# Performance work log

Measured on AMD Instinct MI355X. Metric: run time of the kernel, lower is better.

Reference implementation:

```python
import jax, jax.numpy as jnp
import numpy as np

N_NODES = 50000
N_EDGES = 800000
IN_CH = 256
OUT_CH = 64
HEADS = 4
NEG_SLOPE = 0.2


def setup_inputs() -> dict:
    key = jax.random.key(0)
    k = jax.random.split(key, 7)
    x = jax.random.normal(k[0], (N_NODES, IN_CH), dtype=jnp.float32)
    edge_index = jax.random.randint(k[1], (2, N_EDGES), 0, N_NODES, dtype=jnp.int32)
    # Glorot-style init for the linear projection and attention vectors
    W = jax.random.normal(k[2], (IN_CH, HEADS * OUT_CH), dtype=jnp.float32) / np.sqrt(IN_CH)
    att_src = jax.random.normal(k[3], (HEADS, OUT_CH), dtype=jnp.float32) / np.sqrt(OUT_CH)
    att_dst = jax.random.normal(k[4], (HEADS, OUT_CH), dtype=jnp.float32) / np.sqrt(OUT_CH)
    bias = jnp.zeros((HEADS * OUT_CH,), dtype=jnp.float32)
    return {"x": x, "edge_index": edge_index, "W": W,
            "att_src": att_src, "att_dst": att_dst, "bias": bias}


def reference(x, edge_index, W, att_src, att_dst, bias):
    N = x.shape[0]
    # PyG GATConv default: add self-loops
    loop = jnp.arange(N, dtype=edge_index.dtype)
    src = jnp.concatenate([edge_index[0], loop])
    dst = jnp.concatenate([edge_index[1], loop])

    h = (x @ W).reshape(N, HEADS, OUT_CH)          # [N,H,C]
    a_src = jnp.einsum('nhc,hc->nh', h, att_src)    # [N,H]
    a_dst = jnp.einsum('nhc,hc->nh', h, att_dst)    # [N,H]

    alpha = a_src[src] + a_dst[dst]                 # [E,H]
    alpha = jax.nn.leaky_relu(alpha, NEG_SLOPE)

    # segment softmax over edges grouped by destination node
    amax = jax.ops.segment_max(alpha, dst, num_segments=N)
    amax = jnp.where(jnp.isfinite(amax), amax, 0.0)
    e = jnp.exp(alpha - amax[dst])
    denom = jax.ops.segment_sum(e, dst, num_segments=N)
    coef = e / (denom[dst] + 1e-16)                 # [E,H]

    msg = coef[..., None] * h[src]                  # [E,H,C]
    out = jax.ops.segment_sum(msg, dst, num_segments=N)  # [N,H,C]
    out = out.reshape(N, HEADS * OUT_CH) + bias
    return jax.nn.relu(out)
```

## Files before the change

### kernel.cpp

```cpp
#include <hip/hip_runtime.h>
#include <hip/hip_bf16.h>

#define HC 256
#define NEG_SLOPE 0.2f
#define BM 64
#define BK 64
#define LDK 72

typedef short short8_t __attribute__((ext_vector_type(8)));
typedef float float4_t __attribute__((ext_vector_type(4)));

__device__ __forceinline__ unsigned short f2bf(float f) {
  unsigned u = __float_as_uint(f);
  return (unsigned short)((u + 0x7fffu + ((u >> 16) & 1u)) >> 16);
}
__device__ __forceinline__ float bf2f(unsigned short b) {
  return __uint_as_float(((unsigned)b) << 16);
}

__global__ void wt_kernel(const float* __restrict__ W, unsigned short* __restrict__ Wt)
{
  const int k = blockIdx.x;
  const int n = threadIdx.x;
  Wt[n * 256 + k] = f2bf(W[k * 256 + n]);
}

__global__ __launch_bounds__(256) void gemm_mfma(
    const float* __restrict__ x, const unsigned short* __restrict__ Wt,
    const float* __restrict__ att_src, const float* __restrict__ att_dst,
    unsigned short* __restrict__ h, float* __restrict__ a_src,
    float* __restrict__ a_dst, int nnodes)
{
  __shared__ unsigned short As[BM * LDK];
  __shared__ unsigned short Bs[256 * LDK];
  const int t    = threadIdx.x;
  const int wv   = t >> 6;
  const int lane = t & 63;
  const int r0   = blockIdx.x * BM;

  float4_t acc[4][4] = {};

  for (int k0 = 0; k0 < 256; k0 += BK) {
    __syncthreads();
    {
      const int row = t >> 2, kc = (t & 3) * 16;
      const int gr = r0 + row;
      float4 xv[4];
      if (gr < nnodes) {
        const float4* p = (const float4*)(x + (size_t)gr * 256 + k0 + kc);
        xv[0] = p[0]; xv[1] = p[1]; xv[2] = p[2]; xv[3] = p[3];
      } else {
        xv[0] = xv[1] = xv[2] = xv[3] = make_float4(0.f, 0.f, 0.f, 0.f);
      }
      const float* f = (const float*)xv;
      unsigned pk[8];
      #pragma unroll
      for (int i = 0; i < 8; ++i) {
        __hip_bfloat162 b2 = __float22bfloat162_rn(make_float2(f[2 * i], f[2 * i + 1]));
        pk[i] = *(unsigned*)&b2;
      }
      uint4* d = (uint4*)&As[row * LDK + kc];
      d[0] = make_uint4(pk[0], pk[1], pk[2], pk[3]);
      d[1] = make_uint4(pk[4], pk[5], pk[6], pk[7]);
    }
    #pragma unroll
    for (int it = 0; it < 4; ++it) {
      const int n = it * 64 + (t >> 2);
      const int kc = (t & 3) * 16;
      const uint4* g = (const uint4*)(Wt + (size_t)n * 256 + k0 + kc);
      uint4 v0 = g[0], v1 = g[1];
      uint4* d = (uint4*)&Bs[n * LDK + kc];
      d[0] = v0; d[1] = v1;
    }
    __syncthreads();

    #pragma unroll
    for (int ks = 0; ks < 2; ++ks) {
      const int ko = ks * 32 + (lane >> 4) * 8;
      short8_t af[4], bfr[4];
      #pragma unroll
      for (int mt = 0; mt < 4; ++mt)
        af[mt] = *(const short8_t*)&As[(16 * mt + (lane & 15)) * LDK + ko];
      #pragma unroll
      for (int nt = 0; nt < 4; ++nt)
        bfr[nt] = *(const short8_t*)&Bs[(64 * wv + 16 * nt + (lane & 15)) * LDK + ko];
      #pragma unroll
      for (int mt = 0; mt < 4; ++mt)
        #pragma unroll
        for (int nt = 0; nt < 4; ++nt)
          acc[mt][nt] = __builtin_amdgcn_mfma_f32_16x16x32_bf16(
              af[mt], bfr[nt], acc[mt][nt], 0, 0, 0);
    }
  }

  const int q = lane >> 4, l15 = lane & 15;
  float atts[4], attd[4];
  #pragma unroll
  for (int nt = 0; nt < 4; ++nt) {
    atts[nt] = att_src[wv * 64 + 16 * nt + l15];
    attd[nt] = att_dst[wv * 64 + 16 * nt + l15];
  }

  #pragma unroll
  for (int mt = 0; mt < 4; ++mt) {
    #pragma unroll
    for (int reg = 0; reg < 4; ++reg) {
      const int row = r0 + 16 * mt + 4 * q + reg;
      const bool ok = row < nnodes;
      float ps = 0.f, pd = 0.f;
      #pragma unroll
      for (int nt = 0; nt < 4; ++nt) {
        const float v = acc[mt][nt][reg];
        if (ok) h[(size_t)row * 256 + 64 * wv + 16 * nt + l15] = f2bf(v);
        ps += v * atts[nt];
        pd += v * attd[nt];
      }
      #pragma unroll
      for (int off = 8; off; off >>= 1) {
        ps += __shfl_down(ps, off, 16);
        pd += __shfl_down(pd, off, 16);
      }
      if (ok && l15 == 0) {
        a_src[row * 4 + wv] = ps;
        a_dst[row * 4 + wv] = pd;
      }
    }
  }
}

__global__ void deg_count(const int* __restrict__ ei, int* __restrict__ deg, int E)
{
  const int e = blockIdx.x * blockDim.x + threadIdx.x;
  if (e >= E) return;
  atomicAdd(&deg[ei[E + e]], 1);
}

__global__ __launch_bounds__(256) void scan_p1(const int* __restrict__ deg,
                                               int* __restrict__ bsum, int n)
{
  __shared__ int ws[4];
  const int t = threadIdx.x, lane = t & 63, wv = t >> 6;
  const int base = blockIdx.x * 1024 + t * 4;
  int4 v = make_int4(0, 0, 0, 0);
  if (base + 3 < n) v = *(const int4*)&deg[base];
  else {
    if (base + 0 < n) v.x = deg[base + 0];
    if (base + 1 < n) v.y = deg[base + 1];
    if (base + 2 < n) v.z = deg[base + 2];
  }
  int s = (v.x + v.y) + (v.z + v.w);
  #pragma unroll
  for (int off = 32; off; off >>= 1) s += __shfl_down(s, off, 64);
  if (lane == 0) ws[wv] = s;
  __syncthreads();
  if (t == 0) bsum[blockIdx.x] = (ws[0] + ws[1]) + (ws[2] + ws[3]);
}

__global__ __launch_bounds__(1024) void scan_p2(const int* __restrict__ bsum,
                                                int* __restrict__ boff,
                                                int* __restrict__ rowptr,
                                                int nb, int n)
{
  __shared__ int wsum[16], woff[16];
  const int t = threadIdx.x, lane = t & 63, wv = t >> 6;
  int v = (t < nb) ? bsum[t] : 0;
  int sc = v;
  #pragma unroll
  for (int off = 1; off < 64; off <<= 1) {
    int u = __shfl_up(sc, off, 64);
    if (lane >= off) sc += u;
  }
  if (lane == 63) wsum[wv] = sc;
  __syncthreads();
  if (t == 0) {
    int run = 0;
    #pragma unroll
    for (int i = 0; i < 16; ++i) { int x = wsum[i]; woff[i] = run; run += x; }
    rowptr[n] = run;
  }
  __syncthreads();
  if (t < nb) boff[t] = woff[wv] + sc - v;
}

__global__ __launch_bounds__(256) void scan_p3(const int* __restrict__ deg,
                                               const int* __restrict__ boff,
                                               int* __restrict__ rowptr,
                                               int* __restrict__ cursor, int n)
{
  __shared__ int wsum[4], woff[4];
  const int t = threadIdx.x, lane = t & 63, wv = t >> 6;
  const int base = blockIdx.x * 1024 + t * 4;
  int4 v = make_int4(0, 0, 0, 0);
  if (base + 3 < n) v = *(const int4*)&deg[base];
  else {
    if (base + 0 < n) v.x = deg[base + 0];
    if (base + 1 < n) v.y = deg[base + 1];
    if (base + 2 < n) v.z = deg[base + 2];
  }
  const int s = (v.x + v.y) + (v.z + v.w);
  int sc = s;
  #pragma unroll
  for (int off = 1; off < 64; off <<= 1) {
    int u = __shfl_up(sc, off, 64);
    if (lane >= off) sc += u;
  }
  if (lane == 63) wsum[wv] = sc;
  __syncthreads();
  if (t == 0) {
    int run = 0;
    #pragma unroll
    for (int i = 0; i < 4; ++i) { int x = wsum[i]; woff[i] = run; run += x; }
  }
  __syncthreads();
  int excl = boff[blockIdx.x] + woff[wv] + (sc - s);
  int4 r;
  r.x = excl;
  r.y = r.x + v.x;
  r.z = r.y + v.y;
  r.w = r.z + v.z;
  if (base + 3 < n) {
    *(int4*)&rowptr[base] = r;
    *(int4*)&cursor[base] = r;
  } else {
    if (base + 0 < n) { rowptr[base + 0] = r.x; cursor[base + 0] = r.x; }
    if (base + 1 < n) { rowptr[base + 1] = r.y; cursor[base + 1] = r.y; }
    if (base + 2 < n) { rowptr[base + 2] = r.z; cursor[base + 2] = r.z; }
  }
}

__global__ __launch_bounds__(256) void fill_csr(
    const int* __restrict__ ei, const float* __restrict__ a_src,
    const float* __restrict__ a_dst, int* __restrict__ cursor,
    int* __restrict__ csr_src, float4* __restrict__ wexp, int E, int nnodes)
{
  const int g    = blockIdx.x & 7;
  const int bg   = blockIdx.x >> 3;
  const int nbg  = gridDim.x >> 3;
  const int gsz  = (nnodes + 7) >> 3;
  const int dlo  = g * gsz;
  const int dhi  = min(dlo + gsz, nnodes);

  for (int e = bg * 256 + threadIdx.x; e < E; e += nbg * 256) {
    const int d = ei[E + e];
    if (d < dlo || d >= dhi) continue;
    const int s = ei[e];
    const int pos = atomicAdd(&cursor[d], 1);
    csr_src[pos] = s;
    const float4 as = ((const float4*)a_src)[s];
    const float4 ad = ((const float4*)a_dst)[d];
    float4 al;
    al.x = as.x + ad.x; al.y = as.y + ad.y;
    al.z = as.z + ad.z; al.w = as.w + ad.w;
    al.x = al.x > 0.f ? al.x : NEG_SLOPE * al.x;
    al.y = al.y > 0.f ? al.y : NEG_SLOPE * al.y;
    al.z = al.z > 0.f ? al.z : NEG_SLOPE * al.z;
    al.w = al.w > 0.f ? al.w : NEG_SLOPE * al.w;
    al.x = expf(al.x); al.y = expf(al.y); al.z = expf(al.z); al.w = expf(al.w);
    wexp[pos] = al;
  }
}

__device__ __forceinline__ float4 ld_h(const unsigned short* __restrict__ h,
                                       int row, int cb)
{
  const ushort4 u = *(const ushort4*)&h[(size_t)row * 256 + cb];
  return make_float4(bf2f(u.x), bf2f(u.y), bf2f(u.z), bf2f(u.w));
}

__global__ __launch_bounds__(256) void gather_kernel(
    const int* __restrict__ rowptr, const int* __restrict__ csr_src,
    const float* __restrict__ wexp, const unsigned short* __restrict__ h,
    const float* __restrict__ a_src, const float* __restrict__ a_dst,
    const float* __restrict__ bias, float* __restrict__ out, int n)
{
  const int wave = threadIdx.x >> 6;
  const int lane = threadIdx.x & 63;
  const int d = blockIdx.x * 4 + wave;
  if (d >= n) return;

  const int head = lane >> 4;
  const int cb   = lane * 4;

  float alpha = a_src[d * 4 + head] + a_dst[d * 4 + head];
  alpha = alpha > 0.f ? alpha : NEG_SLOPE * alpha;
  float w = expf(alpha);
  float dsum = w;
  float4 hv = ld_h(h, d, cb);
  float4 acc = make_float4(w * hv.x, w * hv.y, w * hv.z, w * hv.w);

  int j = rowptr[d];
  const int end = rowptr[d + 1];

  for (; j + 3 < end; j += 4) {
    const int4 s4 = *(const int4*)&csr_src[j];
    const float w0 = wexp[(j + 0) * 4 + head];
    const float w1 = wexp[(j + 1) * 4 + head];
    const float w2 = wexp[(j + 2) * 4 + head];
    const float w3 = wexp[(j + 3) * 4 + head];
    const float4 h0 = ld_h(h, s4.x, cb);
    const float4 h1 = ld_h(h, s4.y, cb);
    const float4 h2 = ld_h(h, s4.z, cb);
    const float4 h3 = ld_h(h, s4.w, cb);
    dsum += (w0 + w1) + (w2 + w3);
    acc.x += w0 * h0.x + w1 * h1.x + w2 * h2.x + w3 * h3.x;
    acc.y += w0 * h0.y + w1 * h1.y + w2 * h2.y + w3 * h3.y;
    acc.z += w0 * h0.z + w1 * h1.z + w2 * h2.z + w3 * h3.z;
    acc.w += w0 * h0.w + w1 * h1.w + w2 * h2.w + w3 * h3.w;
  }
  for (; j < end; ++j) {
    const int s0 = csr_src[j];
    const float w0 = wexp[j * 4 + head];
    const float4 h0 = ld_h(h, s0, cb);
    dsum += w0;
    acc.x += w0 * h0.x; acc.y += w0 * h0.y;
    acc.z += w0 * h0.z; acc.w += w0 * h0.w;
  }

  const float inv = 1.f / (dsum + 1e-16f);
  const float4 b4 = ((const float4*)bias)[lane];
  float4 o;
  o.x = acc.x * inv + b4.x; o.x = o.x > 0.f ? o.x : 0.f;
  o.y = acc.y * inv + b4.y; o.y = o.y > 0.f ? o.y : 0.f;
  o.z = acc.z * inv + b4.z; o.z = o.z > 0.f ? o.z : 0.f;
  o.w = acc.w * inv + b4.w; o.w = o.w > 0.f ? o.w : 0.f;
  *(float4*)&out[(size_t)d * 256 + cb] = o;
}

extern "C" void kernel_launch(void* const* d_in, const int* in_sizes, int n_in,
                              void* d_out, int out_size, void* d_ws, size_t ws_size,
                              hipStream_t stream)
{
  const float* x       = (const float*)d_in[0];
  const int*   ei      = (const int*)d_in[1];
  const float* W       = (const float*)d_in[2];
  const float* att_src = (const float*)d_in[3];
  const float* att_dst = (const float*)d_in[4];
  const float* bias    = (const float*)d_in[5];

  const int nnodes = in_sizes[0] / HC;
  const int E      = in_sizes[1] / 2;
  const int nb     = (nnodes + 1023) / 1024;

  float* out = (float*)d_out;
  char* ws = (char*)d_ws;
  unsigned short* h  = (unsigned short*)ws;
  float* a_src = (float*)(ws + (size_t)nnodes * HC * 2);
  float* a_dst = a_src + (size_t)nnodes * 4;
  unsigned short* Wt = (unsigned short*)(a_dst + (size_t)nnodes * 4);
  int* deg    = (int*)((char*)Wt + 256 * 256 * 2);
  int* rowptr = deg + nnodes;
  int* cursor = rowptr + ((nnodes + 1 + 3) & ~3);
  int* bsum   = cursor + nnodes;
  int* boff   = bsum + ((nb + 3) & ~3);
  float4* wexp = (float4*)(boff + ((nb + 3) & ~3));
  int* csr    = (int*)(wexp + E);

  hipMemsetAsync(deg, 0, (size_t)nnodes * sizeof(int), stream);

  wt_kernel<<<256, 256, 0, stream>>>(W, Wt);

  gemm_mfma<<<(nnodes + BM - 1) / BM, 256, 0, stream>>>(
      x, Wt, att_src, att_dst, h, a_src, a_dst, nnodes);

  deg_count<<<(E + 255) / 256, 256, 0, stream>>>(ei, deg, E);
  scan_p1<<<nb, 256, 0, stream>>>(deg, bsum, nnodes);
  scan_p2<<<1, 1024, 0, stream>>>(bsum, boff, rowptr, nb, nnodes);
  scan_p3<<<nb, 256, 0, stream>>>(deg, boff, rowptr, cursor, nnodes);

  fill_csr<<<1024, 256, 0, stream>>>(ei, a_src, a_dst, cursor, csr,
                                     (float4*)wexp, E, nnodes);

  gather_kernel<<<(nnodes + 3) / 4, 256, 0, stream>>>(
      rowptr, csr, (const float*)wexp, h, a_src, a_dst, bias, out, nnodes);
}
```

Baseline: 276.7 us.

## Fuse degree count into GEMM launch, enlarge GEMM tile, vectorize CSR fill and unroll gather

```diff
diff --git a/kernel.cpp b/kernel.cpp
--- a/kernel.cpp
+++ b/kernel.cpp
@@ -3,7 +3,7 @@
 
 #define HC 256
 #define NEG_SLOPE 0.2f
-#define BM 64
+#define BM 128
 #define BK 64
 #define LDK 72
 
@@ -25,43 +25,62 @@
   Wt[n * 256 + k] = f2bf(W[k * 256 + n]);
 }
 
-__global__ __launch_bounds__(256) void gemm_mfma(
+__global__ __launch_bounds__(256) void gemm_deg(
     const float* __restrict__ x, const unsigned short* __restrict__ Wt,
     const float* __restrict__ att_src, const float* __restrict__ att_dst,
     unsigned short* __restrict__ h, float* __restrict__ a_src,
-    float* __restrict__ a_dst, int nnodes)
+    float* __restrict__ a_dst, const int* __restrict__ ei,
+    int* __restrict__ deg, int E, int nnodes, int degBlocks)
 {
   __shared__ unsigned short As[BM * LDK];
   __shared__ unsigned short Bs[256 * LDK];
-  const int t    = threadIdx.x;
+  const int t = threadIdx.x;
+
+  if (blockIdx.x < degBlocks) {
+    const int base = (blockIdx.x * 256 + t) * 4;
+    if (base + 3 < E) {
+      const int4 d4 = *(const int4*)&ei[E + base];
+      atomicAdd(&deg[d4.x], 1);
+      atomicAdd(&deg[d4.y], 1);
+      atomicAdd(&deg[d4.z], 1);
+      atomicAdd(&deg[d4.w], 1);
+    } else {
+      for (int e = base; e < E; ++e) atomicAdd(&deg[ei[E + e]], 1);
+    }
+    return;
+  }
+
   const int wv   = t >> 6;
   const int lane = t & 63;
-  const int r0   = blockIdx.x * BM;
-
-  float4_t acc[4][4] = {};
+  const int r0   = (blockIdx.x - degBlocks) * BM;
+
+  float4_t acc[8][4] = {};
 
   for (int k0 = 0; k0 < 256; k0 += BK) {
     __syncthreads();
     {
-      const int row = t >> 2, kc = (t & 3) * 16;
+      const int row = t >> 1, kc = (t & 1) * 32;
       const int gr = r0 + row;
-      float4 xv[4];
+      float4 xv[8];
       if (gr < nnodes) {
         const float4* p = (const float4*)(x + (size_t)gr * 256 + k0 + kc);
-        xv[0] = p[0]; xv[1] = p[1]; xv[2] = p[2]; xv[3] = p[3];
+        #pragma unroll
+        for (int i = 0; i < 8; ++i) xv[i] = p[i];
       } else {
-        xv[0] = xv[1] = xv[2] = xv[3] = make_float4(0.f, 0.f, 0.f, 0.f);
+        #pragma unroll
+        for (int i = 0; i < 8; ++i) xv[i] = make_float4(0.f, 0.f, 0.f, 0.f);
       }
       const float* f = (const float*)xv;
-      unsigned pk[8];
-      #pragma unroll
-      for (int i = 0; i < 8; ++i) {
+      unsigned pk[16];
+      #pragma unroll
+      for (int i = 0; i < 16; ++i) {
         __hip_bfloat162 b2 = __float22bfloat162_rn(make_float2(f[2 * i], f[2 * i + 1]));
         pk[i] = *(unsigned*)&b2;
       }
       uint4* d = (uint4*)&As[row * LDK + kc];
-      d[0] = make_uint4(pk[0], pk[1], pk[2], pk[3]);
-      d[1] = make_uint4(pk[4], pk[5], pk[6], pk[7]);
+      #pragma unroll
+      for (int i = 0; i < 4; ++i)
+        d[i] = make_uint4(pk[4 * i], pk[4 * i + 1], pk[4 * i + 2], pk[4 * i + 3]);
     }
     #pragma unroll
     for (int it = 0; it < 4; ++it) {
@@ -77,15 +96,15 @@
     #pragma unroll
     for (int ks = 0; ks < 2; ++ks) {
       const int ko = ks * 32 + (lane >> 4) * 8;
-      short8_t af[4], bfr[4];
-      #pragma unroll
-      for (int mt = 0; mt < 4; ++mt)
-        af[mt] = *(const short8_t*)&As[(16 * mt + (lane & 15)) * LDK + ko];
+      short8_t af[8], bfr[4];
       #pragma unroll
       for (int nt = 0; nt < 4; ++nt)
         bfr[nt] = *(const short8_t*)&Bs[(64 * wv + 16 * nt + (lane & 15)) * LDK + ko];
       #pragma unroll
-      for (int mt = 0; mt < 4; ++mt)
+      for (int mt = 0; mt < 8; ++mt)
+        af[mt] = *(const short8_t*)&As[(16 * mt + (lane & 15)) * LDK + ko];
+      #pragma unroll
+      for (int mt = 0; mt < 8; ++mt)
         #pragma unroll
         for (int nt = 0; nt < 4; ++nt)
           acc[mt][nt] = __builtin_amdgcn_mfma_f32_16x16x32_bf16(
@@ -102,7 +121,7 @@
   }
 
   #pragma unroll
-  for (int mt = 0; mt < 4; ++mt) {
+  for (int mt = 0; mt < 8; ++mt) {
     #pragma unroll
     for (int reg = 0; reg < 4; ++reg) {
       const int row = r0 + 16 * mt + 4 * q + reg;
@@ -126,13 +145,6 @@
       }
     }
   }
-}
-
-__global__ void deg_count(const int* __restrict__ ei, int* __restrict__ deg, int E)
-{
-  const int e = blockIdx.x * blockDim.x + threadIdx.x;
-  if (e >= E) return;
-  atomicAdd(&deg[ei[E + e]], 1);
 }
 
 __global__ __launch_bounds__(256) void scan_p1(const int* __restrict__ deg,
@@ -228,6 +240,27 @@
   }
 }
 
+__device__ __forceinline__ void fill_one(
+    int s, int d, int dlo, int dhi, const float* __restrict__ a_src,
+    const float* __restrict__ a_dst, int* __restrict__ cursor,
+    int* __restrict__ csr_src, float4* __restrict__ wexp)
+{
+  if (d < dlo || d >= dhi) return;
+  const int pos = atomicAdd(&cursor[d], 1);
+  csr_src[pos] = s;
+  const float4 as = ((const float4*)a_src)[s];
+  const float4 ad = ((const float4*)a_dst)[d];
+  float4 al;
+  al.x = as.x + ad.x; al.y = as.y + ad.y;
+  al.z = as.z + ad.z; al.w = as.w + ad.w;
+  al.x = al.x > 0.f ? al.x : NEG_SLOPE * al.x;
+  al.y = al.y > 0.f ? al.y : NEG_SLOPE * al.y;
+  al.z = al.z > 0.f ? al.z : NEG_SLOPE * al.z;
+  al.w = al.w > 0.f ? al.w : NEG_SLOPE * al.w;
+  al.x = expf(al.x); al.y = expf(al.y); al.z = expf(al.z); al.w = expf(al.w);
+  wexp[pos] = al;
+}
+
 __global__ __launch_bounds__(256) void fill_csr(
     const int* __restrict__ ei, const float* __restrict__ a_src,
     const float* __restrict__ a_dst, int* __restrict__ cursor,
@@ -239,25 +272,18 @@
   const int gsz  = (nnodes + 7) >> 3;
   const int dlo  = g * gsz;
   const int dhi  = min(dlo + gsz, nnodes);
-
-  for (int e = bg * 256 + threadIdx.x; e < E; e += nbg * 256) {
-    const int d = ei[E + e];
-    if (d < dlo || d >= dhi) continue;
-    const int s = ei[e];
-    const int pos = atomicAdd(&cursor[d], 1);
-    csr_src[pos] = s;
-    const float4 as = ((const float4*)a_src)[s];
-    const float4 ad = ((const float4*)a_dst)[d];
-    float4 al;
-    al.x = as.x + ad.x; al.y = as.y + ad.y;
-    al.z = as.z + ad.z; al.w = as.w + ad.w;
-    al.x = al.x > 0.f ? al.x : NEG_SLOPE * al.x;
-    al.y = al.y > 0.f ? al.y : NEG_SLOPE * al.y;
-    al.z = al.z > 0.f ? al.z : NEG_SLOPE * al.z;
-    al.w = al.w > 0.f ? al.w : NEG_SLOPE * al.w;
-    al.x = expf(al.x); al.y = expf(al.y); al.z = expf(al.z); al.w = expf(al.w);
-    wexp[pos] = al;
-  }
+  const int E4   = E >> 2;
+
+  for (int c = bg * 256 + threadIdx.x; c < E4; c += nbg * 256) {
+    const int4 d4 = *(const int4*)&ei[E + 4 * c];
+    const int4 s4 = *(const int4*)&ei[4 * c];
+    fill_one(s4.x, d4.x, dlo, dhi, a_src, a_dst, cursor, csr_src, wexp);
+    fill_one(s4.y, d4.y, dlo, dhi, a_src, a_dst, cursor, csr_src, wexp);
+    fill_one(s4.z, d4.z, dlo, dhi, a_src, a_dst, cursor, csr_src, wexp);
+    fill_one(s4.w, d4.w, dlo, dhi, a_src, a_dst, cursor, csr_src, wexp);
+  }
+  for (int e = E4 * 4 + bg * 256 + threadIdx.x; e < E; e += nbg * 256)
+    fill_one(ei[e], ei[E + e], dlo, dhi, a_src, a_dst, cursor, csr_src, wexp);
 }
 
 __device__ __forceinline__ float4 ld_h(const unsigned short* __restrict__ h,
@@ -273,9 +299,11 @@
     const float* __restrict__ a_src, const float* __restrict__ a_dst,
     const float* __restrict__ bias, float* __restrict__ out, int n)
 {
+  const int per8 = gridDim.x >> 3;
+  const int vb   = (blockIdx.x & 7) * per8 + (blockIdx.x >> 3);
   const int wave = threadIdx.x >> 6;
   const int lane = threadIdx.x & 63;
-  const int d = blockIdx.x * 4 + wave;
+  const int d = vb * 4 + wave;
   if (d >= n) return;
 
   const int head = lane >> 4;
@@ -291,21 +319,29 @@
   int j = rowptr[d];
   const int end = rowptr[d + 1];
 
-  for (; j + 3 < end; j += 4) {
-    const int4 s4 = *(const int4*)&csr_src[j];
-    const float w0 = wexp[(j + 0) * 4 + head];
-    const float w1 = wexp[(j + 1) * 4 + head];
-    const float w2 = wexp[(j + 2) * 4 + head];
-    const float w3 = wexp[(j + 3) * 4 + head];
-    const float4 h0 = ld_h(h, s4.x, cb);
-    const float4 h1 = ld_h(h, s4.y, cb);
-    const float4 h2 = ld_h(h, s4.z, cb);
-    const float4 h3 = ld_h(h, s4.w, cb);
-    dsum += (w0 + w1) + (w2 + w3);
-    acc.x += w0 * h0.x + w1 * h1.x + w2 * h2.x + w3 * h3.x;
-    acc.y += w0 * h0.y + w1 * h1.y + w2 * h2.y + w3 * h3.y;
-    acc.z += w0 * h0.z + w1 * h1.z + w2 * h2.z + w3 * h3.z;
-    acc.w += w0 * h0.w + w1 * h1.w + w2 * h2.w + w3 * h3.w;
+  for (; j + 7 < end; j += 8) {
+    const int4 sa = *(const int4*)&csr_src[j];
+    const int4 sb = *(const int4*)&csr_src[j + 4];
+    float wj[8];
+    #pragma unroll
+    for (int k = 0; k < 8; ++k) wj[k] = wexp[(j + k) * 4 + head];
+    const float4 h0 = ld_h(h, sa.x, cb);
+    const float4 h1 = ld_h(h, sa.y, cb);
+    const float4 h2 = ld_h(h, sa.z, cb);
+    const float4 h3 = ld_h(h, sa.w, cb);
+    const float4 h4 = ld_h(h, sb.x, cb);
+    const float4 h5 = ld_h(h, sb.y, cb);
+    const float4 h6 = ld_h(h, sb.z, cb);
+    const float4 h7 = ld_h(h, sb.w, cb);
+    dsum += ((wj[0] + wj[1]) + (wj[2] + wj[3])) + ((wj[4] + wj[5]) + (wj[6] + wj[7]));
+    acc.x += wj[0] * h0.x + wj[1] * h1.x + wj[2] * h2.x + wj[3] * h3.x
+           + wj[4] * h4.x + wj[5] * h5.x + wj[6] * h6.x + wj[7] * h7.x;
+    acc.y += wj[0] * h0.y + wj[1] * h1.y + wj[2] * h2.y + wj[3] * h3.y
+           + wj[4] * h4.y + wj[5] * h5.y + wj[6] * h6.y + wj[7] * h7.y;
+    acc.z += wj[0] * h0.z + wj[1] * h1.z + wj[2] * h2.z + wj[3] * h3.z
+           + wj[4] * h4.z + wj[5] * h5.z + wj[6] * h6.z + wj[7] * h7.z;
+    acc.w += wj[0] * h0.w + wj[1] * h1.w + wj[2] * h2.w + wj[3] * h3.w
+           + wj[4] * h4.w + wj[5] * h5.w + wj[6] * h6.w + wj[7] * h7.w;
   }
   for (; j < end; ++j) {
     const int s0 = csr_src[j];
@@ -340,6 +376,9 @@
   const int nnodes = in_sizes[0] / HC;
   const int E      = in_sizes[1] / 2;
   const int nb     = (nnodes + 1023) / 1024;
+  const int degBlocks  = (E + 1023) / 1024;
+  const int gemmBlocks = (nnodes + BM - 1) / BM;
+  const int gatherBlocks = (((nnodes + 3) / 4) + 7) & ~7;
 
   float* out = (float*)d_out;
   char* ws = (char*)d_ws;
@@ -359,10 +398,9 @@
 
   wt_kernel<<<256, 256, 0, stream>>>(W, Wt);
 
-  gemm_mfma<<<(nnodes + BM - 1) / BM, 256, 0, stream>>>(
-      x, Wt, att_src, att_dst, h, a_src, a_dst, nnodes);
-
-  deg_count<<<(E + 255) / 256, 256, 0, stream>>>(ei, deg, E);
+  gemm_deg<<<degBlocks + gemmBlocks, 256, 0, stream>>>(
+      x, Wt, att_src, att_dst, h, a_src, a_dst, ei, deg, E, nnodes, degBlocks);
+
   scan_p1<<<nb, 256, 0, stream>>>(deg, bsum, nnodes);
   scan_p2<<<1, 1024, 0, stream>>>(bsum, boff, rowptr, nb, nnodes);
   scan_p3<<<nb, 256, 0, stream>>>(deg, boff, rowptr, cursor, nnodes);
@@ -370,6 +408,6 @@
   fill_csr<<<1024, 256, 0, stream>>>(ei, a_src, a_dst, cursor, csr,
                                      (float4*)wexp, E, nnodes);
 
-  gather_kernel<<<(nnodes + 3) / 4, 256, 0, stream>>>(
+  gather_kernel<<<gatherBlocks, 256, 0, stream>>>(
       rowptr, csr, (const float*)wexp, h, a_src, a_dst, bias, out, nnodes);
 }
```

Measured after the change: 294.5 us. 6.5% more time.
